# Performance work log

Hardware: AMD Instinct MI355X
Metric: run time of the kernel (lower is better)

The kernel has to match this reference:

```python
import jax, jax.numpy as jnp
import numpy as np

B, N, DEG = 16, 64, 16          # batch, nodes, out-degree per node
IN_F, EDGE_F, OUT_F, H = 1024, 128, 512, 8
F = OUT_F // H                   # n_hidden = 64 (is_concat=True)
E = N * DEG                      # num_edges = 1024
SLOPE = 0.2                      # leaky relu negative slope


def setup_inputs() -> dict:
    key = jax.random.key(0)
    k0, k1, k2, k3, k4 = jax.random.split(key, 5)
    h = jax.random.normal(k0, (B, N, IN_F), dtype=jnp.float32)
    edge_attr = jax.random.normal(k1, (B, E, EDGE_F), dtype=jnp.float32)
    # deterministic adjacency: node i -> nodes (i+k) % N, k=0..DEG-1
    # (includes self-loop, so every softmax row has >=1 neighbor)
    adj = np.zeros((N, N), dtype=np.float32)
    for i in range(N):
        for k in range(DEG):
            adj[i, (i + k) % N] = 1.0
    adj_mat = jnp.asarray(np.broadcast_to(adj, (B, N, N)).copy())
    W_node = jax.random.normal(k2, (IN_F, H * F), dtype=jnp.float32) * 0.03
    W_edge = jax.random.normal(k3, (EDGE_F, H * F), dtype=jnp.float32) * 0.05
    w_attn = jax.random.normal(k4, (3 * F,), dtype=jnp.float32) * 0.1
    return {"h": h, "adj_mat": adj_mat, "edge_attr": edge_attr,
            "W_node": W_node, "W_edge": W_edge, "w_attn": w_attn}


def reference(h, adj_mat, edge_attr, W_node, W_edge, w_attn):
    # node / edge projections
    g = (h @ W_node).reshape(B, N, H, F)                  # [B,N,H,F]
    e_proj = (edge_attr @ W_edge).reshape(B, E, H, F)     # [B,E,H,F]
    # pad edge rows up to N*N (mirrors torch.cat with zero pad)
    e_proj = jnp.pad(e_proj, ((0, 0), (0, N * N - E), (0, 0), (0, 0)))
    # scatter edge features to flattened nonzero adjacency positions,
    # in row-major nonzero order == rank via exclusive cumsum
    idx = adj_mat.reshape(B, N * N).astype(jnp.int32)     # [B,N*N] of 0/1
    rank = jnp.cumsum(idx, axis=1) - idx                  # position among nonzeros
    ef = jnp.take_along_axis(e_proj, rank[:, :, None, None], axis=1)
    ef = ef * idx[:, :, None, None].astype(g.dtype)       # zero where no edge
    ef = ef.reshape(B, N, N, H, F)                        # [B,i,j,H,F]
    # attn(cat[g_i, g_j, edge]) == g_i.w1 + g_j.w2 + edge.w3
    w_i, w_j, w_e = w_attn[:F], w_attn[F:2 * F], w_attn[2 * F:]
    s_i = jnp.einsum('bnhf,f->bnh', g, w_i)
    s_j = jnp.einsum('bnhf,f->bnh', g, w_j)
    s_e = jnp.einsum('bijhf,f->bijh', ef, w_e)
    e = jax.nn.leaky_relu(s_i[:, :, None, :] + s_j[:, None, :, :] + s_e, SLOPE)
    e = jnp.where(adj_mat[..., None] > 0, e, -jnp.inf)    # mask non-edges
    a = jax.nn.softmax(e, axis=2)                         # softmax over j
    # dropout is identity in eval mode
    out = jnp.einsum('bijh,bjhf->bihf', a, g)             # weighted aggregation
    return out.reshape(B, N, H * F)                       # is_concat=True
```

## Files before the change

kernel.cpp:

```cpp
#include <hip/hip_runtime.h>
#include <hip/hip_bf16.h>
#include <stdint.h>

#define BB 16
#define NN 64
#define DEG 16
#define IN_F 1024
#define EDGE_F 128
#define OUT_FT 512
#define HH 8
#define FF 64
#define EE (NN*DEG)
#define SLOPE 0.2f

typedef short s16x8 __attribute__((ext_vector_type(8)));
typedef float f32x4 __attribute__((ext_vector_type(4)));

__device__ __forceinline__ unsigned short f2bf(float x) {
    union { float f; uint32_t u; } v; v.f = x;
    uint32_t u = v.u;
    return (unsigned short)((u + 0x7FFFu + ((u >> 16) & 1u)) >> 16);
}

__global__ __launch_bounds__(256)
void prep_kernel(const float* __restrict__ W_node,
                 const float* __restrict__ W_edge,
                 const float* __restrict__ w_attn,
                 const float* __restrict__ adj,
                 unsigned short* __restrict__ W_T,
                 float* __restrict__ wv,
                 int* __restrict__ row_start)
{
    int bx = blockIdx.x;
    int tid = threadIdx.x;

    if (bx < 128) {
        __shared__ float tile[64][65];
        int tn = bx & 7, tk = bx >> 3;
        int k0 = tk * 64, n0 = tn * 64;
        #pragma unroll
        for (int j = 0; j < 16; ++j) {
            int lin = j * 256 + tid;
            int r = lin >> 6, c = lin & 63;
            tile[r][c] = W_node[(size_t)(k0 + r) * 512 + n0 + c];
        }
        __syncthreads();
        #pragma unroll
        for (int j = 0; j < 16; ++j) {
            int lin = j * 256 + tid;
            int nr = lin >> 6, kc = lin & 63;
            W_T[(size_t)(n0 + nr) * 1024 + k0 + kc] = f2bf(tile[kc][nr]);
        }
    } else if (bx < 144) {
        int b = bx - 128;
        if (tid < 64) {
            const float* row = adj + (size_t)b * 4096 + (size_t)tid * 64;
            int cnt = 0;
            #pragma unroll 8
            for (int j = 0; j < 64; ++j) cnt += (row[j] > 0.5f) ? 1 : 0;
            int inc = cnt;
            #pragma unroll
            for (int d = 1; d < 64; d <<= 1) {
                int u = __shfl_up(inc, d, 64);
                if (tid >= d) inc += u;
            }
            row_start[b * 64 + tid] = inc - cnt;
        }
    } else {
        int c = tid & 127;
        int half = tid >> 7;
        const float* we = w_attn + 2 * FF;
        #pragma unroll
        for (int hh = 0; hh < 4; ++hh) {
            int h = half * 4 + hh;
            float s = 0.f;
            const float* row = W_edge + (size_t)c * 512 + h * 64;
            #pragma unroll 8
            for (int f = 0; f < 64; ++f) s += row[f] * we[f];
            wv[c * 8 + h] = s;
        }
    }
}

__global__ __launch_bounds__(256)
void main_kernel(const float* __restrict__ hmat,
                 const unsigned short* __restrict__ W_T,
                 const float* __restrict__ edge_attr,
                 const float* __restrict__ wv,
                 const float* __restrict__ w_attn,
                 float* __restrict__ g,
                 float* __restrict__ s_e,
                 float* __restrict__ s_i,
                 float* __restrict__ s_j)
{
    __shared__ __align__(16) unsigned short As[2][64][40];
    __shared__ __align__(16) unsigned short Bs[2][64][40];
    __shared__ float wvs[1024];

    int bx = blockIdx.x;
    int tid = threadIdx.x;

    if (bx < 128) {
        int head = bx & 7, mt = bx >> 3;
        int n0 = head * 64, m0 = mt * 64;
        int wave = tid >> 6, lane = tid & 63;
        int l15 = lane & 15, quad = lane >> 4;
        int wv16 = wave * 16;

        int ldr = tid >> 2;
        int ldc8 = (tid & 3) * 8;

        const float* apBase = hmat + (size_t)(m0 + ldr) * 1024 + ldc8;
        const unsigned short* bpBase = W_T + (size_t)(n0 + ldr) * 1024 + ldc8;

        f32x4 acc[4];
        #pragma unroll
        for (int i = 0; i < 4; ++i) acc[i] = (f32x4){0.f, 0.f, 0.f, 0.f};

        float4 a0 = *(const float4*)(apBase);
        float4 a1 = *(const float4*)(apBase + 4);
        int4   bv = *(const int4*)(bpBase);
        {
            s16x8 av;
            av[0] = (short)f2bf(a0.x); av[1] = (short)f2bf(a0.y);
            av[2] = (short)f2bf(a0.z); av[3] = (short)f2bf(a0.w);
            av[4] = (short)f2bf(a1.x); av[5] = (short)f2bf(a1.y);
            av[6] = (short)f2bf(a1.z); av[7] = (short)f2bf(a1.w);
            *(s16x8*)&As[0][ldr][ldc8] = av;
            *(int4*)&Bs[0][ldr][ldc8] = bv;
        }

        for (int it = 0; it < 32; ++it) {
            __syncthreads();
            if (it + 1 < 32) {
                const float* ap = apBase + (it + 1) * 32;
                a0 = *(const float4*)ap;
                a1 = *(const float4*)(ap + 4);
                bv = *(const int4*)(bpBase + (it + 1) * 32);
            }
            int cur = it & 1;
            s16x8 af = *(const s16x8*)&As[cur][wv16 + l15][quad * 8];
            #pragma unroll
            for (int nt = 0; nt < 4; ++nt) {
                s16x8 bf = *(const s16x8*)&Bs[cur][nt * 16 + l15][quad * 8];
                acc[nt] = __builtin_amdgcn_mfma_f32_16x16x32_bf16(af, bf, acc[nt], 0, 0, 0);
            }
            if (it + 1 < 32) {
                int nxt = cur ^ 1;
                s16x8 av;
                av[0] = (short)f2bf(a0.x); av[1] = (short)f2bf(a0.y);
                av[2] = (short)f2bf(a0.z); av[3] = (short)f2bf(a0.w);
                av[4] = (short)f2bf(a1.x); av[5] = (short)f2bf(a1.y);
                av[6] = (short)f2bf(a1.z); av[7] = (short)f2bf(a1.w);
                *(s16x8*)&As[nxt][ldr][ldc8] = av;
                *(int4*)&Bs[nxt][ldr][ldc8] = bv;
            }
        }

        float wi[4], wj[4];
        #pragma unroll
        for (int nt = 0; nt < 4; ++nt) {
            wi[nt] = w_attn[nt * 16 + l15];
            wj[nt] = w_attn[64 + nt * 16 + l15];
        }
        float pi[4], pj[4];
        #pragma unroll
        for (int reg = 0; reg < 4; ++reg) { pi[reg] = 0.f; pj[reg] = 0.f; }

        #pragma unroll
        for (int nt = 0; nt < 4; ++nt) {
            #pragma unroll
            for (int reg = 0; reg < 4; ++reg) {
                int gm = m0 + wv16 + quad * 4 + reg;
                int gn = n0 + nt * 16 + l15;
                g[(size_t)gm * 512 + gn] = acc[nt][reg];
                pi[reg] += acc[nt][reg] * wi[nt];
                pj[reg] += acc[nt][reg] * wj[nt];
            }
        }
        #pragma unroll
        for (int mask = 1; mask < 16; mask <<= 1) {
            #pragma unroll
            for (int reg = 0; reg < 4; ++reg) {
                pi[reg] += __shfl_xor(pi[reg], mask);
                pj[reg] += __shfl_xor(pj[reg], mask);
            }
        }
        if (l15 == 0) {
            #pragma unroll
            for (int reg = 0; reg < 4; ++reg) {
                int r = m0 + wv16 + quad * 4 + reg;
                s_i[(size_t)r * 8 + head] = pi[reg];
                s_j[(size_t)r * 8 + head] = pj[reg];
            }
        }
    } else {
        ((float4*)wvs)[tid] = ((const float4*)wv)[tid];
        __syncthreads();
        int e = (bx - 128) * 256 + tid;
        const float4* erow = (const float4*)(edge_attr + (size_t)e * 128);
        f32x4 accl = {0.f, 0.f, 0.f, 0.f};
        f32x4 acch = {0.f, 0.f, 0.f, 0.f};
        for (int c4 = 0; c4 < 32; ++c4) {
            float4 v = erow[c4];
            #pragma unroll
            for (int u = 0; u < 4; ++u) {
                int c = c4 * 4 + u;
                f32x4 w0 = *(const f32x4*)&wvs[c * 8];
                f32x4 w1 = *(const f32x4*)&wvs[c * 8 + 4];
                float x = (u == 0) ? v.x : (u == 1) ? v.y : (u == 2) ? v.z : v.w;
                accl += x * w0;
                acch += x * w1;
            }
        }
        *(f32x4*)(s_e + (size_t)e * 8)     = accl;
        *(f32x4*)(s_e + (size_t)e * 8 + 4) = acch;
    }
}

__global__ __launch_bounds__(256)
void attn_kernel(const float* __restrict__ g,
                 const float* __restrict__ adj,
                 const float* __restrict__ s_e,
                 const float* __restrict__ s_i,
                 const float* __restrict__ s_j,
                 const int*   __restrict__ row_start,
                 float* __restrict__ out)
{
    __shared__ __align__(16) float gs[16][516];
    __shared__ float se_s[16][8];
    __shared__ float sj_s[16][8];
    __shared__ float a_s[16][8];
    __shared__ float si_s[8];
    __shared__ int nbr[16];
    __shared__ int m_nb_s;

    int bi = blockIdx.x;
    int b = bi >> 6, i = bi & 63;
    int tid = threadIdx.x;

    if (tid < 64) {
        float av = adj[(size_t)b * 4096 + (size_t)i * 64 + tid];
        unsigned long long m = __ballot(av > 0.5f);
        if (av > 0.5f) {
            int before = __popcll(m & ((1ull << tid) - 1ull));
            if (before < 16) nbr[before] = tid;
        }
        if (tid == 0) {
            int c = __popcll(m);
            m_nb_s = (c > 16) ? 16 : c;
        }
    }
    __syncthreads();

    int m_nb = m_nb_s;
    int rs = row_start[bi];

    int slot = tid >> 4, l16 = tid & 15;
    if (slot < m_nb) {
        const float4* src4 = (const float4*)(g + (size_t)(b * 64 + nbr[slot]) * 512);
        #pragma unroll
        for (int j = 0; j < 8; ++j) {
            int q = j * 16 + l16;
            *(float4*)&gs[slot][q * 4] = src4[q];
        }
    }
    if (tid < 128) {
        int k = tid >> 3, h = tid & 7;
        if (k < m_nb) {
            se_s[k][h] = s_e[(size_t)(b * 1024 + rs + k) * 8 + h];
            sj_s[k][h] = s_j[(size_t)(b * 64 + nbr[k]) * 8 + h];
        }
    } else if (tid < 136) {
        si_s[tid - 128] = s_i[(size_t)bi * 8 + (tid - 128)];
    }
    __syncthreads();

    if (tid < 8) {
        int h = tid;
        float si = si_s[h];
        float sc[16];
        float mx = -1e30f;
        for (int k = 0; k < m_nb; ++k) {
            float v = si + sj_s[k][h] + se_s[k][h];
            v = (v >= 0.f) ? v : SLOPE * v;
            sc[k] = v;
            mx = fmaxf(mx, v);
        }
        float ssum = 0.f;
        for (int k = 0; k < m_nb; ++k) {
            float e = __expf(sc[k] - mx);
            a_s[k][h] = e;
            ssum += e;
        }
        float inv = 1.f / ssum;
        for (int k = 0; k < m_nb; ++k) a_s[k][h] *= inv;
    }
    __syncthreads();

    int c0 = tid * 2;
    int h = tid >> 5;
    float a0 = 0.f, a1 = 0.f;
    for (int k = 0; k < m_nb; ++k) {
        float ak = a_s[k][h];
        a0 += ak * gs[k][c0];
        a1 += ak * gs[k][c0 + 1];
    }
    out[(size_t)bi * 512 + c0]     = a0;
    out[(size_t)bi * 512 + c0 + 1] = a1;
}

extern "C" void kernel_launch(void* const* d_in, const int* in_sizes, int n_in,
                              void* d_out, int out_size, void* d_ws, size_t ws_size,
                              hipStream_t stream) {
    const float* h_in      = (const float*)d_in[0];
    const float* adj_mat   = (const float*)d_in[1];
    const float* edge_attr = (const float*)d_in[2];
    const float* W_node    = (const float*)d_in[3];
    const float* W_edge    = (const float*)d_in[4];
    const float* w_attn    = (const float*)d_in[5];
    float* out = (float*)d_out;

    char* ws = (char*)d_ws;
    unsigned short* W_T = (unsigned short*)(ws + 0x000000);
    float* g            = (float*)(ws + 0x100000);
    float* s_e          = (float*)(ws + 0x300000);
    float* s_i          = (float*)(ws + 0x380000);
    float* s_j          = (float*)(ws + 0x388000);
    float* wv           = (float*)(ws + 0x390000);
    int*   row_start    = (int*)  (ws + 0x391000);

    prep_kernel<<<145, 256, 0, stream>>>(W_node, W_edge, w_attn, adj_mat,
                                         W_T, wv, row_start);
    main_kernel<<<192, 256, 0, stream>>>(h_in, W_T, edge_attr, wv, w_attn,
                                         g, s_e, s_i, s_j);
    attn_kernel<<<1024, 256, 0, stream>>>(g, adj_mat, s_e, s_i, s_j,
                                          row_start, out);
}
```

Before: 102.2 us.

## Fuse three kernels into one persistent launch with atomic-counter inter-block dependencies

Merges the prep, projection and attention kernels into a single 592-block launch in which roles are chosen by block index. Dependencies between stages are enforced through global atomic counters and spin-waits, replacing kernel boundaries. The attention stage now handles four rows per block, one wave per row, and reads neighbour g rows straight from global memory instead of staging them in shared memory. Each s_e block recomputes the edge-weight vector itself. The spin-waits assume producer blocks get scheduled before or alongside their consumers, which risks deadlock-like stalls if they are not, and a memset launch is added.

```diff
diff --git a/kernel.cpp b/kernel.cpp
--- a/kernel.cpp
+++ b/kernel.cpp
@@ -2,15 +2,6 @@
 #include <hip/hip_bf16.h>
 #include <stdint.h>
 
-#define BB 16
-#define NN 64
-#define DEG 16
-#define IN_F 1024
-#define EDGE_F 128
-#define OUT_FT 512
-#define HH 8
-#define FF 64
-#define EE (NN*DEG)
 #define SLOPE 0.2f
 
 typedef short s16x8 __attribute__((ext_vector_type(8)));
@@ -22,20 +13,29 @@
     return (unsigned short)((u + 0x7FFFu + ((u >> 16) & 1u)) >> 16);
 }
 
-__global__ __launch_bounds__(256)
-void prep_kernel(const float* __restrict__ W_node,
-                 const float* __restrict__ W_edge,
-                 const float* __restrict__ w_attn,
-                 const float* __restrict__ adj,
-                 unsigned short* __restrict__ W_T,
-                 float* __restrict__ wv,
-                 int* __restrict__ row_start)
+__global__ __launch_bounds__(256, 4)
+void fused_kernel(const float* __restrict__ hmat,
+                  const float* __restrict__ adj,
+                  const float* __restrict__ edge_attr,
+                  const float* __restrict__ W_node,
+                  const float* __restrict__ W_edge,
+                  const float* __restrict__ w_attn,
+                  unsigned short* __restrict__ W_T,
+                  float* __restrict__ g,
+                  float* __restrict__ s_e,
+                  float* __restrict__ s_i,
+                  float* __restrict__ s_j,
+                  int* __restrict__ row_start,
+                  int* __restrict__ cntA,
+                  int* __restrict__ cntB,
+                  float* __restrict__ out)
 {
+    __shared__ __align__(16) char smem[20608];
     int bx = blockIdx.x;
     int tid = threadIdx.x;
 
     if (bx < 128) {
-        __shared__ float tile[64][65];
+        float (*tile)[65] = (float (*)[65])smem;
         int tn = bx & 7, tk = bx >> 3;
         int k0 = tk * 64, n0 = tn * 64;
         #pragma unroll
@@ -51,62 +51,19 @@
             int nr = lin >> 6, kc = lin & 63;
             W_T[(size_t)(n0 + nr) * 1024 + k0 + kc] = f2bf(tile[kc][nr]);
         }
-    } else if (bx < 144) {
-        int b = bx - 128;
-        if (tid < 64) {
-            const float* row = adj + (size_t)b * 4096 + (size_t)tid * 64;
-            int cnt = 0;
-            #pragma unroll 8
-            for (int j = 0; j < 64; ++j) cnt += (row[j] > 0.5f) ? 1 : 0;
-            int inc = cnt;
-            #pragma unroll
-            for (int d = 1; d < 64; d <<= 1) {
-                int u = __shfl_up(inc, d, 64);
-                if (tid >= d) inc += u;
-            }
-            row_start[b * 64 + tid] = inc - cnt;
-        }
-    } else {
-        int c = tid & 127;
-        int half = tid >> 7;
-        const float* we = w_attn + 2 * FF;
-        #pragma unroll
-        for (int hh = 0; hh < 4; ++hh) {
-            int h = half * 4 + hh;
-            float s = 0.f;
-            const float* row = W_edge + (size_t)c * 512 + h * 64;
-            #pragma unroll 8
-            for (int f = 0; f < 64; ++f) s += row[f] * we[f];
-            wv[c * 8 + h] = s;
-        }
-    }
-}
-
-__global__ __launch_bounds__(256)
-void main_kernel(const float* __restrict__ hmat,
-                 const unsigned short* __restrict__ W_T,
-                 const float* __restrict__ edge_attr,
-                 const float* __restrict__ wv,
-                 const float* __restrict__ w_attn,
-                 float* __restrict__ g,
-                 float* __restrict__ s_e,
-                 float* __restrict__ s_i,
-                 float* __restrict__ s_j)
-{
-    __shared__ __align__(16) unsigned short As[2][64][40];
-    __shared__ __align__(16) unsigned short Bs[2][64][40];
-    __shared__ float wvs[1024];
-
-    int bx = blockIdx.x;
-    int tid = threadIdx.x;
-
-    if (bx < 128) {
-        int head = bx & 7, mt = bx >> 3;
+        __threadfence();
+        __syncthreads();
+        if (tid == 0)
+            __hip_atomic_fetch_add(cntA, 1, __ATOMIC_RELEASE, __HIP_MEMORY_SCOPE_AGENT);
+    } else if (bx < 256) {
+        unsigned short* As = (unsigned short*)smem;
+        unsigned short* Bs = (unsigned short*)(smem + 10240);
+        int rb = bx - 128;
+        int head = rb & 7, mt = rb >> 3;
         int n0 = head * 64, m0 = mt * 64;
         int wave = tid >> 6, lane = tid & 63;
         int l15 = lane & 15, quad = lane >> 4;
         int wv16 = wave * 16;
-
         int ldr = tid >> 2;
         int ldc8 = (tid & 3) * 8;
 
@@ -119,15 +76,23 @@
 
         float4 a0 = *(const float4*)(apBase);
         float4 a1 = *(const float4*)(apBase + 4);
-        int4   bv = *(const int4*)(bpBase);
+        if (tid == 0) {
+            int it = 0;
+            while (__hip_atomic_load(cntA, __ATOMIC_ACQUIRE, __HIP_MEMORY_SCOPE_AGENT) < 128
+                   && ++it < (1 << 24))
+                __builtin_amdgcn_s_sleep(2);
+        }
+        __syncthreads();
+
+        int4 bv = *(const int4*)(bpBase);
         {
             s16x8 av;
             av[0] = (short)f2bf(a0.x); av[1] = (short)f2bf(a0.y);
             av[2] = (short)f2bf(a0.z); av[3] = (short)f2bf(a0.w);
             av[4] = (short)f2bf(a1.x); av[5] = (short)f2bf(a1.y);
             av[6] = (short)f2bf(a1.z); av[7] = (short)f2bf(a1.w);
-            *(s16x8*)&As[0][ldr][ldc8] = av;
-            *(int4*)&Bs[0][ldr][ldc8] = bv;
+            *(s16x8*)&As[ldr * 40 + ldc8] = av;
+            *(int4*)&Bs[ldr * 40 + ldc8] = bv;
         }
 
         for (int it = 0; it < 32; ++it) {
@@ -139,21 +104,21 @@
                 bv = *(const int4*)(bpBase + (it + 1) * 32);
             }
             int cur = it & 1;
-            s16x8 af = *(const s16x8*)&As[cur][wv16 + l15][quad * 8];
+            s16x8 af = *(const s16x8*)&As[(cur * 64 + wv16 + l15) * 40 + quad * 8];
             #pragma unroll
             for (int nt = 0; nt < 4; ++nt) {
-                s16x8 bf = *(const s16x8*)&Bs[cur][nt * 16 + l15][quad * 8];
+                s16x8 bf = *(const s16x8*)&Bs[(cur * 64 + nt * 16 + l15) * 40 + quad * 8];
                 acc[nt] = __builtin_amdgcn_mfma_f32_16x16x32_bf16(af, bf, acc[nt], 0, 0, 0);
             }
             if (it + 1 < 32) {
-                int nxt = cur ^ 1;
+                int nxt = (it & 1) ^ 1;
                 s16x8 av;
                 av[0] = (short)f2bf(a0.x); av[1] = (short)f2bf(a0.y);
                 av[2] = (short)f2bf(a0.z); av[3] = (short)f2bf(a0.w);
                 av[4] = (short)f2bf(a1.x); av[5] = (short)f2bf(a1.y);
                 av[6] = (short)f2bf(a1.z); av[7] = (short)f2bf(a1.w);
-                *(s16x8*)&As[nxt][ldr][ldc8] = av;
-                *(int4*)&Bs[nxt][ldr][ldc8] = bv;
+                *(s16x8*)&As[(nxt * 64 + ldr) * 40 + ldc8] = av;
+                *(int4*)&Bs[(nxt * 64 + ldr) * 40 + ldc8] = bv;
             }
         }
 
@@ -166,7 +131,6 @@
         float pi[4], pj[4];
         #pragma unroll
         for (int reg = 0; reg < 4; ++reg) { pi[reg] = 0.f; pj[reg] = 0.f; }
-
         #pragma unroll
         for (int nt = 0; nt < 4; ++nt) {
             #pragma unroll
@@ -194,10 +158,27 @@
                 s_j[(size_t)r * 8 + head] = pj[reg];
             }
         }
-    } else {
-        ((float4*)wvs)[tid] = ((const float4*)wv)[tid];
-        __syncthreads();
-        int e = (bx - 128) * 256 + tid;
+        __threadfence();
+        __syncthreads();
+        if (tid == 0)
+            __hip_atomic_fetch_add(cntB, 1, __ATOMIC_RELEASE, __HIP_MEMORY_SCOPE_AGENT);
+    } else if (bx < 320) {
+        float* wvs = (float*)smem;
+        {
+            int c = tid & 127, half = tid >> 7;
+            const float* we = w_attn + 128;
+            #pragma unroll
+            for (int hh = 0; hh < 4; ++hh) {
+                int h = half * 4 + hh;
+                float s = 0.f;
+                const float* row = W_edge + (size_t)c * 512 + h * 64;
+                #pragma unroll 8
+                for (int f = 0; f < 64; ++f) s += row[f] * we[f];
+                wvs[c * 8 + h] = s;
+            }
+        }
+        __syncthreads();
+        int e = (bx - 256) * 256 + tid;
         const float4* erow = (const float4*)(edge_attr + (size_t)e * 128);
         f32x4 accl = {0.f, 0.f, 0.f, 0.f};
         f32x4 acch = {0.f, 0.f, 0.f, 0.f};
@@ -215,99 +196,97 @@
         }
         *(f32x4*)(s_e + (size_t)e * 8)     = accl;
         *(f32x4*)(s_e + (size_t)e * 8 + 4) = acch;
+        __threadfence();
+        __syncthreads();
+        if (tid == 0)
+            __hip_atomic_fetch_add(cntB, 1, __ATOMIC_RELEASE, __HIP_MEMORY_SCOPE_AGENT);
+    } else if (bx < 336) {
+        int b = bx - 320;
+        if (tid < 64) {
+            const float* row = adj + (size_t)b * 4096 + (size_t)tid * 64;
+            int cnt = 0;
+            #pragma unroll 8
+            for (int j = 0; j < 64; ++j) cnt += (row[j] > 0.5f) ? 1 : 0;
+            int inc = cnt;
+            #pragma unroll
+            for (int d = 1; d < 64; d <<= 1) {
+                int u = __shfl_up(inc, d, 64);
+                if (tid >= d) inc += u;
+            }
+            row_start[b * 64 + tid] = inc - cnt;
+        }
+        __threadfence();
+        __syncthreads();
+        if (tid == 0)
+            __hip_atomic_fetch_add(cntB, 1, __ATOMIC_RELEASE, __HIP_MEMORY_SCOPE_AGENT);
+    } else {
+        float* a_s = (float*)smem;
+        int*   nbr = (int*)(smem + 2048);
+        int bi4 = bx - 336;
+        int b = bi4 >> 4;
+        int i = (bi4 & 15) * 4 + (tid >> 6);
+        int w = tid >> 6, lane = tid & 63;
+        int bi = b * 64 + i;
+
+        float av = adj[(size_t)b * 4096 + (size_t)i * 64 + lane];
+        unsigned long long m = __ballot(av > 0.5f);
+        int m_nb = __popcll(m); m_nb = (m_nb > 16) ? 16 : m_nb;
+        int r = __popcll(m & ((1ull << lane) - 1ull));
+        if ((av > 0.5f) && r < 16) nbr[w * 16 + r] = lane;
+
+        if (tid == 0) {
+            int it = 0;
+            while (__hip_atomic_load(cntB, __ATOMIC_ACQUIRE, __HIP_MEMORY_SCOPE_AGENT) < 208
+                   && ++it < (1 << 24))
+                __builtin_amdgcn_s_sleep(2);
+        }
+        __syncthreads();
+
+        int rs = row_start[bi];
+
+        int k = lane & 15, g2 = lane >> 4;
+        int h0 = g2 * 2, h1 = h0 + 1;
+        float sc0 = -1e30f, sc1 = -1e30f;
+        int jn = nbr[w * 16 + k];
+        if (k < m_nb) {
+            float v0 = s_i[(size_t)bi * 8 + h0] + s_j[(size_t)(b * 64 + jn) * 8 + h0]
+                     + s_e[(size_t)(b * 1024 + rs + k) * 8 + h0];
+            float v1 = s_i[(size_t)bi * 8 + h1] + s_j[(size_t)(b * 64 + jn) * 8 + h1]
+                     + s_e[(size_t)(b * 1024 + rs + k) * 8 + h1];
+            sc0 = (v0 >= 0.f) ? v0 : SLOPE * v0;
+            sc1 = (v1 >= 0.f) ? v1 : SLOPE * v1;
+        }
+        float mx0 = sc0, mx1 = sc1;
+        #pragma unroll
+        for (int mask = 1; mask < 16; mask <<= 1) {
+            mx0 = fmaxf(mx0, __shfl_xor(mx0, mask));
+            mx1 = fmaxf(mx1, __shfl_xor(mx1, mask));
+        }
+        float e0 = (k < m_nb) ? __expf(sc0 - mx0) : 0.f;
+        float e1 = (k < m_nb) ? __expf(sc1 - mx1) : 0.f;
+        float t0 = e0, t1 = e1;
+        #pragma unroll
+        for (int mask = 1; mask < 16; mask <<= 1) {
+            t0 += __shfl_xor(t0, mask);
+            t1 += __shfl_xor(t1, mask);
+        }
+        a_s[(w * 16 + k) * 8 + h0] = e0 / t0;
+        a_s[(w * 16 + k) * 8 + h1] = e1 / t1;
+
+        int c0 = lane * 8;
+        int h = lane >> 3;
+        f32x4 o0 = {0.f, 0.f, 0.f, 0.f};
+        f32x4 o1 = {0.f, 0.f, 0.f, 0.f};
+        for (int kk = 0; kk < m_nb; ++kk) {
+            float ak = a_s[(w * 16 + kk) * 8 + h];
+            int jj = nbr[w * 16 + kk];
+            const f32x4* gr = (const f32x4*)(g + (size_t)(b * 64 + jj) * 512 + c0);
+            o0 += ak * gr[0];
+            o1 += ak * gr[1];
+        }
+        *(f32x4*)(out + (size_t)bi * 512 + c0)     = o0;
+        *(f32x4*)(out + (size_t)bi * 512 + c0 + 4) = o1;
     }
-}
-
-__global__ __launch_bounds__(256)
-void attn_kernel(const float* __restrict__ g,
-                 const float* __restrict__ adj,
-                 const float* __restrict__ s_e,
-                 const float* __restrict__ s_i,
-                 const float* __restrict__ s_j,
-                 const int*   __restrict__ row_start,
-                 float* __restrict__ out)
-{
-    __shared__ __align__(16) float gs[16][516];
-    __shared__ float se_s[16][8];
-    __shared__ float sj_s[16][8];
-    __shared__ float a_s[16][8];
-    __shared__ float si_s[8];
-    __shared__ int nbr[16];
-    __shared__ int m_nb_s;
-
-    int bi = blockIdx.x;
-    int b = bi >> 6, i = bi & 63;
-    int tid = threadIdx.x;
-
-    if (tid < 64) {
-        float av = adj[(size_t)b * 4096 + (size_t)i * 64 + tid];
-        unsigned long long m = __ballot(av > 0.5f);
-        if (av > 0.5f) {
-            int before = __popcll(m & ((1ull << tid) - 1ull));
-            if (before < 16) nbr[before] = tid;
-        }
-        if (tid == 0) {
-            int c = __popcll(m);
-            m_nb_s = (c > 16) ? 16 : c;
-        }
-    }
-    __syncthreads();
-
-    int m_nb = m_nb_s;
-    int rs = row_start[bi];
-
-    int slot = tid >> 4, l16 = tid & 15;
-    if (slot < m_nb) {
-        const float4* src4 = (const float4*)(g + (size_t)(b * 64 + nbr[slot]) * 512);
-        #pragma unroll
-        for (int j = 0; j < 8; ++j) {
-            int q = j * 16 + l16;
-            *(float4*)&gs[slot][q * 4] = src4[q];
-        }
-    }
-    if (tid < 128) {
-        int k = tid >> 3, h = tid & 7;
-        if (k < m_nb) {
-            se_s[k][h] = s_e[(size_t)(b * 1024 + rs + k) * 8 + h];
-            sj_s[k][h] = s_j[(size_t)(b * 64 + nbr[k]) * 8 + h];
-        }
-    } else if (tid < 136) {
-        si_s[tid - 128] = s_i[(size_t)bi * 8 + (tid - 128)];
-    }
-    __syncthreads();
-
-    if (tid < 8) {
-        int h = tid;
-        float si = si_s[h];
-        float sc[16];
-        float mx = -1e30f;
-        for (int k = 0; k < m_nb; ++k) {
-            float v = si + sj_s[k][h] + se_s[k][h];
-            v = (v >= 0.f) ? v : SLOPE * v;
-            sc[k] = v;
-            mx = fmaxf(mx, v);
-        }
-        float ssum = 0.f;
-        for (int k = 0; k < m_nb; ++k) {
-            float e = __expf(sc[k] - mx);
-            a_s[k][h] = e;
-            ssum += e;
-        }
-        float inv = 1.f / ssum;
-        for (int k = 0; k < m_nb; ++k) a_s[k][h] *= inv;
-    }
-    __syncthreads();
-
-    int c0 = tid * 2;
-    int h = tid >> 5;
-    float a0 = 0.f, a1 = 0.f;
-    for (int k = 0; k < m_nb; ++k) {
-        float ak = a_s[k][h];
-        a0 += ak * gs[k][c0];
-        a1 += ak * gs[k][c0 + 1];
-    }
-    out[(size_t)bi * 512 + c0]     = a0;
-    out[(size_t)bi * 512 + c0 + 1] = a1;
 }
 
 extern "C" void kernel_launch(void* const* d_in, const int* in_sizes, int n_in,
@@ -327,13 +306,12 @@
     float* s_e          = (float*)(ws + 0x300000);
     float* s_i          = (float*)(ws + 0x380000);
     float* s_j          = (float*)(ws + 0x388000);
-    float* wv           = (float*)(ws + 0x390000);
-    int*   row_start    = (int*)  (ws + 0x391000);
-
-    prep_kernel<<<145, 256, 0, stream>>>(W_node, W_edge, w_attn, adj_mat,
-                                         W_T, wv, row_start);
-    main_kernel<<<192, 256, 0, stream>>>(h_in, W_T, edge_attr, wv, w_attn,
-                                         g, s_e, s_i, s_j);
-    attn_kernel<<<1024, 256, 0, stream>>>(g, adj_mat, s_e, s_i, s_j,
-                                          row_start, out);
+    int*   row_start    = (int*)  (ws + 0x390000);
+    int*   flags        = (int*)  (ws + 0x3A0000);
+
+    hipMemsetAsync(flags, 0, 64, stream);
+    fused_kernel<<<592, 256, 0, stream>>>(h_in, adj_mat, edge_attr,
+                                          W_node, W_edge, w_attn,
+                                          W_T, g, s_e, s_i, s_j, row_start,
+                                          flags, flags + 1, out);
 }
```

Result: slower. 279.1 us (+173.1%).

## Fuse prep kernel into main kernel, transposing W_node on the fly

Applied to the files above, without the earlier changes.

Removes the separate prep kernel. The GEMM blocks now read fp32 W_node directly and convert and transpose it into LDS as packed bf16 pairs. The edge-score blocks compute the W_edge·w_e vector themselves, and extra blocks compute the adjacency row prefix sums. This saves one launch and the round trip of writing and re-reading W_T, at the cost of reading fp32 weights (twice the bytes), scattered 32-bit LDS stores, and redundant wv computation in each of the 64 edge blocks.

```diff
diff --git a/kernel.cpp b/kernel.cpp
--- a/kernel.cpp
+++ b/kernel.cpp
@@ -2,15 +2,6 @@
 #include <hip/hip_bf16.h>
 #include <stdint.h>
 
-#define BB 16
-#define NN 64
-#define DEG 16
-#define IN_F 1024
-#define EDGE_F 128
-#define OUT_FT 512
-#define HH 8
-#define FF 64
-#define EE (NN*DEG)
 #define SLOPE 0.2f
 
 typedef short s16x8 __attribute__((ext_vector_type(8)));
@@ -23,82 +14,24 @@
 }
 
 __global__ __launch_bounds__(256)
-void prep_kernel(const float* __restrict__ W_node,
+void main_kernel(const float* __restrict__ hmat,
+                 const float* __restrict__ adj,
+                 const float* __restrict__ edge_attr,
+                 const float* __restrict__ W_node,
                  const float* __restrict__ W_edge,
-                 const float* __restrict__ w_attn,
-                 const float* __restrict__ adj,
-                 unsigned short* __restrict__ W_T,
-                 float* __restrict__ wv,
-                 int* __restrict__ row_start)
-{
-    int bx = blockIdx.x;
-    int tid = threadIdx.x;
-
-    if (bx < 128) {
-        __shared__ float tile[64][65];
-        int tn = bx & 7, tk = bx >> 3;
-        int k0 = tk * 64, n0 = tn * 64;
-        #pragma unroll
-        for (int j = 0; j < 16; ++j) {
-            int lin = j * 256 + tid;
-            int r = lin >> 6, c = lin & 63;
-            tile[r][c] = W_node[(size_t)(k0 + r) * 512 + n0 + c];
-        }
-        __syncthreads();
-        #pragma unroll
-        for (int j = 0; j < 16; ++j) {
-            int lin = j * 256 + tid;
-            int nr = lin >> 6, kc = lin & 63;
-            W_T[(size_t)(n0 + nr) * 1024 + k0 + kc] = f2bf(tile[kc][nr]);
-        }
-    } else if (bx < 144) {
-        int b = bx - 128;
-        if (tid < 64) {
-            const float* row = adj + (size_t)b * 4096 + (size_t)tid * 64;
-            int cnt = 0;
-            #pragma unroll 8
-            for (int j = 0; j < 64; ++j) cnt += (row[j] > 0.5f) ? 1 : 0;
-            int inc = cnt;
-            #pragma unroll
-            for (int d = 1; d < 64; d <<= 1) {
-                int u = __shfl_up(inc, d, 64);
-                if (tid >= d) inc += u;
-            }
-            row_start[b * 64 + tid] = inc - cnt;
-        }
-    } else {
-        int c = tid & 127;
-        int half = tid >> 7;
-        const float* we = w_attn + 2 * FF;
-        #pragma unroll
-        for (int hh = 0; hh < 4; ++hh) {
-            int h = half * 4 + hh;
-            float s = 0.f;
-            const float* row = W_edge + (size_t)c * 512 + h * 64;
-            #pragma unroll 8
-            for (int f = 0; f < 64; ++f) s += row[f] * we[f];
-            wv[c * 8 + h] = s;
-        }
-    }
-}
-
-__global__ __launch_bounds__(256)
-void main_kernel(const float* __restrict__ hmat,
-                 const unsigned short* __restrict__ W_T,
-                 const float* __restrict__ edge_attr,
-                 const float* __restrict__ wv,
                  const float* __restrict__ w_attn,
                  float* __restrict__ g,
                  float* __restrict__ s_e,
                  float* __restrict__ s_i,
-                 float* __restrict__ s_j)
+                 float* __restrict__ s_j,
+                 int* __restrict__ row_start)
 {
-    __shared__ __align__(16) unsigned short As[2][64][40];
-    __shared__ __align__(16) unsigned short Bs[2][64][40];
-    __shared__ float wvs[1024];
-
-    int bx = blockIdx.x;
-    int tid = threadIdx.x;
+    __shared__ __align__(16) char U[20480];
+    unsigned short* As = (unsigned short*)U;
+    unsigned short* Bs = (unsigned short*)(U + 10240);
+    float* wvs = (float*)U;
+
+    int bx = blockIdx.x, tid = threadIdx.x;
 
     if (bx < 128) {
         int head = bx & 7, mt = bx >> 3;
@@ -107,11 +40,11 @@
         int l15 = lane & 15, quad = lane >> 4;
         int wv16 = wave * 16;
 
-        int ldr = tid >> 2;
-        int ldc8 = (tid & 3) * 8;
+        int ldr = tid >> 2, ldc8 = (tid & 3) * 8;
+        int kp = tid >> 4, nq = tid & 15;
 
         const float* apBase = hmat + (size_t)(m0 + ldr) * 1024 + ldc8;
-        const unsigned short* bpBase = W_T + (size_t)(n0 + ldr) * 1024 + ldc8;
+        const float* bpBase = W_node + (size_t)(2 * kp) * 512 + n0 + nq * 4;
 
         f32x4 acc[4];
         #pragma unroll
@@ -119,15 +52,21 @@
 
         float4 a0 = *(const float4*)(apBase);
         float4 a1 = *(const float4*)(apBase + 4);
-        int4   bv = *(const int4*)(bpBase);
+        float4 b0 = *(const float4*)(bpBase);
+        float4 b1 = *(const float4*)(bpBase + 512);
         {
             s16x8 av;
             av[0] = (short)f2bf(a0.x); av[1] = (short)f2bf(a0.y);
             av[2] = (short)f2bf(a0.z); av[3] = (short)f2bf(a0.w);
             av[4] = (short)f2bf(a1.x); av[5] = (short)f2bf(a1.y);
             av[6] = (short)f2bf(a1.z); av[7] = (short)f2bf(a1.w);
-            *(s16x8*)&As[0][ldr][ldc8] = av;
-            *(int4*)&Bs[0][ldr][ldc8] = bv;
+            *(s16x8*)&As[ldr * 40 + ldc8] = av;
+            const float* p0 = &b0.x; const float* p1 = &b1.x;
+            #pragma unroll
+            for (int u = 0; u < 4; ++u) {
+                uint32_t pk = (uint32_t)f2bf(p0[u]) | ((uint32_t)f2bf(p1[u]) << 16);
+                *(uint32_t*)&Bs[(nq * 4 + u) * 40 + 2 * kp] = pk;
+            }
         }
 
         for (int it = 0; it < 32; ++it) {
@@ -136,13 +75,15 @@
                 const float* ap = apBase + (it + 1) * 32;
                 a0 = *(const float4*)ap;
                 a1 = *(const float4*)(ap + 4);
-                bv = *(const int4*)(bpBase + (it + 1) * 32);
+                const float* bp = bpBase + (size_t)(it + 1) * 32 * 512;
+                b0 = *(const float4*)bp;
+                b1 = *(const float4*)(bp + 512);
             }
             int cur = it & 1;
-            s16x8 af = *(const s16x8*)&As[cur][wv16 + l15][quad * 8];
+            s16x8 af = *(const s16x8*)&As[(cur * 64 + wv16 + l15) * 40 + quad * 8];
             #pragma unroll
             for (int nt = 0; nt < 4; ++nt) {
-                s16x8 bf = *(const s16x8*)&Bs[cur][nt * 16 + l15][quad * 8];
+                s16x8 bf = *(const s16x8*)&Bs[(cur * 64 + nt * 16 + l15) * 40 + quad * 8];
                 acc[nt] = __builtin_amdgcn_mfma_f32_16x16x32_bf16(af, bf, acc[nt], 0, 0, 0);
             }
             if (it + 1 < 32) {
@@ -152,8 +93,13 @@
                 av[2] = (short)f2bf(a0.z); av[3] = (short)f2bf(a0.w);
                 av[4] = (short)f2bf(a1.x); av[5] = (short)f2bf(a1.y);
                 av[6] = (short)f2bf(a1.z); av[7] = (short)f2bf(a1.w);
-                *(s16x8*)&As[nxt][ldr][ldc8] = av;
-                *(int4*)&Bs[nxt][ldr][ldc8] = bv;
+                *(s16x8*)&As[(nxt * 64 + ldr) * 40 + ldc8] = av;
+                const float* p0 = &b0.x; const float* p1 = &b1.x;
+                #pragma unroll
+                for (int u = 0; u < 4; ++u) {
+                    uint32_t pk = (uint32_t)f2bf(p0[u]) | ((uint32_t)f2bf(p1[u]) << 16);
+                    *(uint32_t*)&Bs[(nxt * 64 + nq * 4 + u) * 40 + 2 * kp] = pk;
+                }
             }
         }
 
@@ -166,7 +112,6 @@
         float pi[4], pj[4];
         #pragma unroll
         for (int reg = 0; reg < 4; ++reg) { pi[reg] = 0.f; pj[reg] = 0.f; }
-
         #pragma unroll
         for (int nt = 0; nt < 4; ++nt) {
             #pragma unroll
@@ -194,8 +139,20 @@
                 s_j[(size_t)r * 8 + head] = pj[reg];
             }
         }
-    } else {
-        ((float4*)wvs)[tid] = ((const float4*)wv)[tid];
+    } else if (bx < 192) {
+        {
+            int c = tid & 127, half = tid >> 7;
+            const float* we = w_attn + 128;
+            #pragma unroll
+            for (int hh = 0; hh < 4; ++hh) {
+                int h = half * 4 + hh;
+                float s = 0.f;
+                const float* row = W_edge + (size_t)c * 512 + h * 64;
+                #pragma unroll 8
+                for (int f = 0; f < 64; ++f) s += row[f] * we[f];
+                wvs[c * 8 + h] = s;
+            }
+        }
         __syncthreads();
         int e = (bx - 128) * 256 + tid;
         const float4* erow = (const float4*)(edge_attr + (size_t)e * 128);
@@ -215,6 +172,21 @@
         }
         *(f32x4*)(s_e + (size_t)e * 8)     = accl;
         *(f32x4*)(s_e + (size_t)e * 8 + 4) = acch;
+    } else {
+        int b = bx - 192;
+        if (tid < 64) {
+            const float* row = adj + (size_t)b * 4096 + (size_t)tid * 64;
+            int cnt = 0;
+            #pragma unroll 8
+            for (int j = 0; j < 64; ++j) cnt += (row[j] > 0.5f) ? 1 : 0;
+            int inc = cnt;
+            #pragma unroll
+            for (int d = 1; d < 64; d <<= 1) {
+                int u = __shfl_up(inc, d, 64);
+                if (tid >= d) inc += u;
+            }
+            row_start[b * 64 + tid] = inc - cnt;
+        }
     }
 }
 
@@ -322,18 +294,15 @@
     float* out = (float*)d_out;
 
     char* ws = (char*)d_ws;
-    unsigned short* W_T = (unsigned short*)(ws + 0x000000);
-    float* g            = (float*)(ws + 0x100000);
-    float* s_e          = (float*)(ws + 0x300000);
-    float* s_i          = (float*)(ws + 0x380000);
-    float* s_j          = (float*)(ws + 0x388000);
-    float* wv           = (float*)(ws + 0x390000);
-    int*   row_start    = (int*)  (ws + 0x391000);
-
-    prep_kernel<<<145, 256, 0, stream>>>(W_node, W_edge, w_attn, adj_mat,
-                                         W_T, wv, row_start);
-    main_kernel<<<192, 256, 0, stream>>>(h_in, W_T, edge_attr, wv, w_attn,
-                                         g, s_e, s_i, s_j);
+    float* g         = (float*)(ws + 0x000000);
+    float* s_e       = (float*)(ws + 0x200000);
+    float* s_i       = (float*)(ws + 0x280000);
+    float* s_j       = (float*)(ws + 0x288000);
+    int*   row_start = (int*)  (ws + 0x290000);
+
+    main_kernel<<<208, 256, 0, stream>>>(h_in, adj_mat, edge_attr,
+                                         W_node, W_edge, w_attn,
+                                         g, s_e, s_i, s_j, row_start);
     attn_kernel<<<1024, 256, 0, stream>>>(g, adj_mat, s_e, s_i, s_j,
                                           row_start, out);
 }
```

Result: faster. 97.45 us (-4.6%).
